# Performance work log

Measured on AMD Instinct MI355X. Metric: run time of the kernel, lower is better.

The kernel has to match this reference:

```python
import jax, jax.numpy as jnp
import numpy as np

N_HEADS = 16

def setup_inputs() -> dict:
    key = jax.random.key(0)
    ks = jax.random.split(key, 5)
    B, T, C = 4, 2048, 1024
    s = 0.02
    return {
        "x": jax.random.normal(ks[0], (B, T, C), jnp.float32),
        "W_attn": jax.random.normal(ks[1], (C, 3 * C), jnp.float32) * s,
        "b_attn": jax.random.normal(ks[2], (3 * C,), jnp.float32) * s,
        "W_proj": jax.random.normal(ks[3], (C, C), jnp.float32) * s,
        "b_proj": jax.random.normal(ks[4], (C,), jnp.float32) * s,
    }

def reference(x, W_attn, b_attn, W_proj, b_proj):
    B, T, C = x.shape
    H = N_HEADS
    D = C // H  # head dim
    qkv = x @ W_attn + b_attn                      # [B,T,3C]
    q, k, v = jnp.split(qkv, 3, axis=2)
    # [B,T,C] -> [B,H,T,D]
    q = q.reshape(B, T, H, D).transpose(0, 2, 1, 3)
    k = k.reshape(B, T, H, D).transpose(0, 2, 1, 3)
    v = v.reshape(B, T, H, D).transpose(0, 2, 1, 3)
    scale = 1.0 / jnp.sqrt(jnp.asarray(D, q.dtype))
    attn = jnp.einsum("bhqd,bhkd->bhqk", q, k) * scale  # [B,H,T,T]
    causal = jnp.tril(jnp.ones((T, T), bool))
    attn = jnp.where(causal[None, None], attn, -jnp.inf)
    attn = jax.nn.softmax(attn, axis=-1)
    y = jnp.einsum("bhqk,bhkd->bhqd", attn, v)          # [B,H,T,D]
    y = y.transpose(0, 2, 1, 3).reshape(B, T, C)
    return y @ W_proj + b_proj
```

## Files before the change

### kernel.cpp

```cpp
#include <hip/hip_runtime.h>

typedef __bf16 bf16x8 __attribute__((ext_vector_type(8)));
typedef float f32x4 __attribute__((ext_vector_type(4)));
typedef float f32x16 __attribute__((ext_vector_type(16)));
typedef unsigned short ushort8 __attribute__((ext_vector_type(8)));
typedef unsigned int uint4v __attribute__((ext_vector_type(4)));

__device__ __forceinline__ unsigned short f2bf(float f) {
  __bf16 b = (__bf16)f;
  return __builtin_bit_cast(unsigned short, b);
}

__global__ __launch_bounds__(256) void wtrans_kernel(const float* __restrict__ W,
                                                     __bf16* __restrict__ Wt,
                                                     int K, int N) {
  __shared__ float tile[32][33];
  int tx = threadIdx.x, ty = threadIdx.y;
  int n0 = blockIdx.x * 32, k0 = blockIdx.y * 32;
#pragma unroll
  for (int i = 0; i < 32; i += 8)
    tile[ty + i][tx] = W[(size_t)(k0 + ty + i) * N + n0 + tx];
  __syncthreads();
#pragma unroll
  for (int i = 0; i < 32; i += 8)
    Wt[(size_t)(n0 + ty + i) * K + k0 + tx] = (__bf16)tile[tx][ty + i];
}

template <int A_F32, int OUT_F32>
__global__ __launch_bounds__(256) void gemm_bt_kernel(const void* __restrict__ Ap,
                                                      const __bf16* __restrict__ Bt,
                                                      const float* __restrict__ bias,
                                                      void* __restrict__ Cp,
                                                      int M, int N, int K) {
  __shared__ __align__(16) unsigned short As[128][40];
  __shared__ __align__(16) unsigned short Bs[128][40];
  const int tid = threadIdx.x;
  const int lane = tid & 63;
  const int wid = tid >> 6;
  const int lr = lane & 15, lg = lane >> 4;
  const int m0 = blockIdx.y * 128, n0 = blockIdx.x * 128;
  const int wm = (wid >> 1) * 64, wn = (wid & 1) * 64;
  f32x4 acc[4][4] = {};
  for (int k0 = 0; k0 < K; k0 += 32) {
#pragma unroll
    for (int p = 0; p < 2; ++p) {
      int idx = p * 256 + tid;
      int r = idx >> 2, c8 = (idx & 3) * 8;
      if (A_F32) {
        const float* A = (const float*)Ap;
        const float4* s4 = (const float4*)(A + (size_t)(m0 + r) * K + k0 + c8);
        float4 f0 = s4[0], f1 = s4[1];
        ushort8 u = {f2bf(f0.x), f2bf(f0.y), f2bf(f0.z), f2bf(f0.w),
                     f2bf(f1.x), f2bf(f1.y), f2bf(f1.z), f2bf(f1.w)};
        *(ushort8*)&As[r][c8] = u;
      } else {
        const __bf16* A = (const __bf16*)Ap;
        *(ushort8*)&As[r][c8] = *(const ushort8*)(A + (size_t)(m0 + r) * K + k0 + c8);
      }
      *(ushort8*)&Bs[r][c8] = *(const ushort8*)(Bt + (size_t)(n0 + r) * K + k0 + c8);
    }
    __syncthreads();
    bf16x8 af[4], bfr[4];
#pragma unroll
    for (int i = 0; i < 4; ++i) af[i] = *(const bf16x8*)&As[wm + i * 16 + lr][lg * 8];
#pragma unroll
    for (int i = 0; i < 4; ++i) bfr[i] = *(const bf16x8*)&Bs[wn + i * 16 + lr][lg * 8];
#pragma unroll
    for (int i = 0; i < 4; ++i)
#pragma unroll
      for (int jn = 0; jn < 4; ++jn)
        acc[i][jn] = __builtin_amdgcn_mfma_f32_16x16x32_bf16(af[i], bfr[jn], acc[i][jn], 0, 0, 0);
    __syncthreads();
  }
#pragma unroll
  for (int i = 0; i < 4; ++i)
#pragma unroll
    for (int jn = 0; jn < 4; ++jn)
#pragma unroll
      for (int jj = 0; jj < 4; ++jj) {
        int row = m0 + wm + i * 16 + lg * 4 + jj;
        int col = n0 + wn + jn * 16 + lr;
        float v = acc[i][jn][jj] + bias[col];
        if (OUT_F32)
          ((float*)Cp)[(size_t)row * N + col] = v;
        else
          ((unsigned short*)Cp)[(size_t)row * N + col] = f2bf(v);
      }
}

__global__ __launch_bounds__(256) void reshape_qk_kernel(const __bf16* __restrict__ qkv,
                                                         __bf16* __restrict__ Q,
                                                         __bf16* __restrict__ Ko) {
  int tid = blockIdx.x * 256 + threadIdx.x;
  int d8 = tid & 7;
  int t = (tid >> 3) & 2047;
  int h = (tid >> 14) & 15;
  int b = tid >> 18;
  size_t src = (size_t)(b * 2048 + t) * 3072 + h * 64 + d8 * 8;
  size_t dst = (size_t)((b * 16 + h) * 2048 + t) * 64 + d8 * 8;
  *(ushort8*)((unsigned short*)Q + dst) = *(const ushort8*)((const unsigned short*)qkv + src);
  *(ushort8*)((unsigned short*)Ko + dst) =
      *(const ushort8*)((const unsigned short*)qkv + src + 1024);
}

__global__ __launch_bounds__(256) void vtrans_kernel(const __bf16* __restrict__ qkv,
                                                     __bf16* __restrict__ Vt) {
  __shared__ __align__(16) unsigned short tile[64][72];
  int bh = blockIdx.y, b = bh >> 4, h = bh & 15;
  int t0 = blockIdx.x * 64;
  int tid = threadIdx.x;
#pragma unroll
  for (int p = 0; p < 2; ++p) {
    int idx = p * 256 + tid;
    int r = idx >> 3, c8 = (idx & 7) * 8;
    *(ushort8*)&tile[r][c8] = *(const ushort8*)((const unsigned short*)qkv +
                                                (size_t)(b * 2048 + t0 + r) * 3072 + 2048 +
                                                h * 64 + c8);
  }
  __syncthreads();
#pragma unroll
  for (int p = 0; p < 2; ++p) {
    int idx = p * 256 + tid;
    int d = idx >> 3, c8 = (idx & 7) * 8;
    ushort8 u;
#pragma unroll
    for (int i = 0; i < 8; ++i) u[i] = tile[c8 + i][d];
    *(ushort8*)((unsigned short*)Vt + (size_t)(bh * 64 + d) * 2048 + t0 + c8) = u;
  }
}

__global__ __launch_bounds__(256) void attn_kernel(const __bf16* __restrict__ Q,
                                                   const __bf16* __restrict__ Kg,
                                                   const __bf16* __restrict__ Vt,
                                                   __bf16* __restrict__ yb) {
  __shared__ __align__(16) unsigned short Ks[2][64][72];
  __shared__ __align__(16) unsigned short Vs[2][64][72];
  const int bx = blockIdx.x;
  const int qb = 15 - (bx >> 6);
  const int bh = bx & 63;
  const int b = bh >> 4, h = bh & 15;
  const int tid = threadIdx.x, wid = tid >> 6, lane = tid & 63;
  const int lq = lane & 31, hi = lane >> 5;
  const unsigned short* Qh = (const unsigned short*)Q + (size_t)bh * 2048 * 64;
  const unsigned short* Kh = (const unsigned short*)Kg + (size_t)bh * 2048 * 64;
  const unsigned short* Vh = (const unsigned short*)Vt + (size_t)bh * 64 * 2048;
  const int q0w = qb * 128 + wid * 32;
  const int jmax_w = 2 * qb + (wid >> 1);
  const int qrel = (wid & 1) * 32 + lq;
  const int J = 2 * qb + 2;

  bf16x8 qf[4];
#pragma unroll
  for (int dc = 0; dc < 4; ++dc)
    qf[dc] = *(const bf16x8*)(Qh + (size_t)(q0w + lq) * 64 + dc * 16 + hi * 8);

  f32x16 yacc[2] = {};
  float m_r = -1e30f, l_r = 0.f;
  const float sc = 0.125f * 1.44269504f;

  {
#pragma unroll
    for (int p = 0; p < 2; ++p) {
      int idx = p * 256 + tid;
      int r = idx >> 3, c8 = (idx & 7) * 8;
      *(ushort8*)&Ks[0][r][c8] = *(const ushort8*)(Kh + (size_t)r * 64 + c8);
      *(ushort8*)&Vs[0][r][c8] = *(const ushort8*)(Vh + (size_t)r * 2048 + c8);
    }
  }

  for (int j = 0; j < J; ++j) {
    __syncthreads();
    if (j + 1 < J) {
      int bi = (j + 1) & 1;
#pragma unroll
      for (int p = 0; p < 2; ++p) {
        int idx = p * 256 + tid;
        int r = idx >> 3, c8 = (idx & 7) * 8;
        *(ushort8*)&Ks[bi][r][c8] =
            *(const ushort8*)(Kh + (size_t)((j + 1) * 64 + r) * 64 + c8);
        *(ushort8*)&Vs[bi][r][c8] =
            *(const ushort8*)(Vh + (size_t)r * 2048 + (j + 1) * 64 + c8);
      }
    }
    if (j <= jmax_w) {
      const int cb = j & 1;
      f32x16 sa[2];
#pragma unroll
      for (int kt32 = 0; kt32 < 2; ++kt32) {
        f32x16 s = {};
#pragma unroll
        for (int dc = 0; dc < 4; ++dc) {
          bf16x8 kf = *(const bf16x8*)&Ks[cb][kt32 * 32 + lq][dc * 16 + hi * 8];
          s = __builtin_amdgcn_mfma_f32_32x32x16_bf16(kf, qf[dc], s, 0, 0, 0);
        }
        sa[kt32] = s;
      }
      float pmax = -1e30f;
#pragma unroll
      for (int kt32 = 0; kt32 < 2; ++kt32)
#pragma unroll
        for (int reg = 0; reg < 16; ++reg) {
          float v = sa[kt32][reg] * sc;
          int kl = kt32 * 32 + (reg & 3) + 8 * (reg >> 2) + 4 * hi;
          if (j == jmax_w && kl > qrel) v = -1e30f;
          sa[kt32][reg] = v;
          pmax = fmaxf(pmax, v);
        }
      pmax = fmaxf(pmax, __shfl_xor(pmax, 32));
      const bool need = __any(pmax > m_r + 8.f) != 0;
      const float mnew = need ? fmaxf(m_r, pmax) : m_r;
      const float alpha = exp2f(m_r - mnew);
      unsigned int u[2][8];
      float rs = 0.f;
#pragma unroll
      for (int kt32 = 0; kt32 < 2; ++kt32)
#pragma unroll
        for (int r = 0; r < 8; ++r) {
          float p0 = exp2f(sa[kt32][2 * r] - mnew);
          float p1 = exp2f(sa[kt32][2 * r + 1] - mnew);
          rs += p0 + p1;
          unsigned int up;
          asm("v_cvt_pk_bf16_f32 %0, %1, %2" : "=v"(up) : "v"(p0), "v"(p1));
          u[kt32][r] = up;
        }
      rs += __shfl_xor(rs, 32);
      l_r = l_r * alpha + rs;
      m_r = mnew;
      if (need) {
#pragma unroll
        for (int reg = 0; reg < 16; ++reg) {
          int row = (reg & 3) + 8 * (reg >> 2) + 4 * hi;
          float ac = __shfl(alpha, row);
          yacc[0][reg] *= ac;
          yacc[1][reg] *= ac;
        }
      }
#pragma unroll
      for (int kt = 0; kt < 4; ++kt) {
        const int kt32 = kt >> 1, off = 4 * (kt & 1);
        unsigned int a0 = u[kt32][off + 0], a2 = u[kt32][off + 2];
        unsigned int a1 = u[kt32][off + 1], a3 = u[kt32][off + 3];
        asm("v_permlane32_swap_b32 %0, %1" : "+v"(a0), "+v"(a2));
        asm("v_permlane32_swap_b32 %0, %1" : "+v"(a1), "+v"(a3));
        uint4v pav = {a0, a1, a2, a3};
        bf16x8 paf = __builtin_bit_cast(bf16x8, pav);
#pragma unroll
        for (int dt = 0; dt < 2; ++dt) {
          bf16x8 vf = *(const bf16x8*)&Vs[cb][dt * 32 + lq][kt * 16 + hi * 8];
          yacc[dt] = __builtin_amdgcn_mfma_f32_32x32x16_bf16(paf, vf, yacc[dt], 0, 0, 0);
        }
      }
    }
  }
#pragma unroll
  for (int reg = 0; reg < 16; ++reg) {
    int row = (reg & 3) + 8 * (reg >> 2) + 4 * hi;
    float linv = 1.f / __shfl(l_r, row);
    int qg = q0w + row;
#pragma unroll
    for (int dt = 0; dt < 2; ++dt) {
      float v = yacc[dt][reg] * linv;
      ((unsigned short*)yb)[(size_t)(b * 2048 + qg) * 1024 + h * 64 + dt * 32 + lq] = f2bf(v);
    }
  }
}

extern "C" void kernel_launch(void* const* d_in, const int* in_sizes, int n_in,
                              void* d_out, int out_size, void* d_ws, size_t ws_size,
                              hipStream_t stream) {
  const float* x = (const float*)d_in[0];
  const float* W_attn = (const float*)d_in[1];
  const float* b_attn = (const float*)d_in[2];
  const float* W_proj = (const float*)d_in[3];
  const float* b_proj = (const float*)d_in[4];
  float* out = (float*)d_out;
  char* ws = (char*)d_ws;

  size_t off = 0;
  __bf16* WtA = (__bf16*)(ws + off); off += (size_t)3072 * 1024 * 2;
  __bf16* WtP = (__bf16*)(ws + off); off += (size_t)1024 * 1024 * 2;
  __bf16* qkv = (__bf16*)(ws + off); off += (size_t)8192 * 3072 * 2;
  __bf16* Qb  = (__bf16*)(ws + off); off += (size_t)64 * 2048 * 64 * 2;
  __bf16* Kb  = (__bf16*)(ws + off); off += (size_t)64 * 2048 * 64 * 2;
  __bf16* Vtb = (__bf16*)(ws + off); off += (size_t)64 * 2048 * 64 * 2;
  __bf16* yb  = (__bf16*)(ws + off); off += (size_t)8192 * 1024 * 2;
  (void)ws_size; (void)in_sizes; (void)n_in; (void)out_size;

  wtrans_kernel<<<dim3(3072 / 32, 1024 / 32), dim3(32, 8), 0, stream>>>(W_attn, WtA, 1024, 3072);
  wtrans_kernel<<<dim3(1024 / 32, 1024 / 32), dim3(32, 8), 0, stream>>>(W_proj, WtP, 1024, 1024);
  gemm_bt_kernel<1, 0><<<dim3(24, 64), 256, 0, stream>>>(x, WtA, b_attn, qkv, 8192, 3072, 1024);
  reshape_qk_kernel<<<4096, 256, 0, stream>>>(qkv, Qb, Kb);
  vtrans_kernel<<<dim3(32, 64), 256, 0, stream>>>(qkv, Vtb);
  attn_kernel<<<dim3(1024), 256, 0, stream>>>(Qb, Kb, Vtb, yb);
  gemm_bt_kernel<0, 1><<<dim3(8, 64), 256, 0, stream>>>(yb, WtP, b_proj, out, 8192, 1024, 1024);
}
```

Measured before the change: 219.0 us.

## Pre-convert x to bf16 and load GEMM tiles directly into LDS

Adds a separate kernel that converts x to bf16 ahead of time, so both GEMMs read bf16 A operands. The GEMM then stages A and B tiles with global_load_lds direct-to-LDS loads instead of going through registers, and remaps block IDs so neighbouring workgroups spread across XCDs for better L2 locality. The LDS tiles lose their padding, which can cause bank conflicts on fragment reads. The extra conversion pass also costs another read and write of x, and the buffer is shared with y.

```diff
diff --git a/kernel.cpp b/kernel.cpp
--- a/kernel.cpp
+++ b/kernel.cpp
@@ -9,6 +9,21 @@
 __device__ __forceinline__ unsigned short f2bf(float f) {
   __bf16 b = (__bf16)f;
   return __builtin_bit_cast(unsigned short, b);
+}
+
+#define GLOAD_LDS16(g, l)                                              \
+  __builtin_amdgcn_global_load_lds(                                    \
+      (const __attribute__((address_space(1))) void*)(g),              \
+      (__attribute__((address_space(3))) void*)(l), 16, 0, 0)
+
+__global__ __launch_bounds__(256) void f32_to_bf16_kernel(const float* __restrict__ in,
+                                                          __bf16* __restrict__ out) {
+  int i = blockIdx.x * 256 + threadIdx.x;
+  const float4* p = (const float4*)(in + (size_t)i * 8);
+  float4 f0 = p[0], f1 = p[1];
+  ushort8 u = {f2bf(f0.x), f2bf(f0.y), f2bf(f0.z), f2bf(f0.w),
+               f2bf(f1.x), f2bf(f1.y), f2bf(f1.z), f2bf(f1.w)};
+  *(ushort8*)((unsigned short*)out + (size_t)i * 8) = u;
 }
 
 __global__ __launch_bounds__(256) void wtrans_kernel(const float* __restrict__ W,
@@ -26,45 +41,42 @@
     Wt[(size_t)(n0 + ty + i) * K + k0 + tx] = (__bf16)tile[tx][ty + i];
 }
 
-template <int A_F32, int OUT_F32>
-__global__ __launch_bounds__(256) void gemm_bt_kernel(const void* __restrict__ Ap,
+template <int OUT_F32>
+__global__ __launch_bounds__(256) void gemm_bt_kernel(const __bf16* __restrict__ Ab,
                                                       const __bf16* __restrict__ Bt,
                                                       const float* __restrict__ bias,
                                                       void* __restrict__ Cp,
                                                       int M, int N, int K) {
-  __shared__ __align__(16) unsigned short As[128][40];
-  __shared__ __align__(16) unsigned short Bs[128][40];
+  __shared__ __align__(16) unsigned short As[128 * 32];
+  __shared__ __align__(16) unsigned short Bs[128 * 32];
   const int tid = threadIdx.x;
   const int lane = tid & 63;
   const int wid = tid >> 6;
   const int lr = lane & 15, lg = lane >> 4;
-  const int m0 = blockIdx.y * 128, n0 = blockIdx.x * 128;
+  const int gx = gridDim.x;
+  int nwg = gx * gridDim.y;
+  int bid = blockIdx.y * gx + blockIdx.x;
+  if ((nwg & 7) == 0) {
+    int cpx = nwg >> 3;
+    bid = (bid & 7) * cpx + (bid >> 3);
+  }
+  const int m0 = (bid / gx) * 128, n0 = (bid % gx) * 128;
   const int wm = (wid >> 1) * 64, wn = (wid & 1) * 64;
+  const int sr = tid >> 2, sc = (tid & 3) * 8;
+  const unsigned short* Ag = (const unsigned short*)Ab + (size_t)(m0 + sr) * K + sc;
+  const unsigned short* Bg = (const unsigned short*)Bt + (size_t)(n0 + sr) * K + sc;
   f32x4 acc[4][4] = {};
   for (int k0 = 0; k0 < K; k0 += 32) {
-#pragma unroll
-    for (int p = 0; p < 2; ++p) {
-      int idx = p * 256 + tid;
-      int r = idx >> 2, c8 = (idx & 3) * 8;
-      if (A_F32) {
-        const float* A = (const float*)Ap;
-        const float4* s4 = (const float4*)(A + (size_t)(m0 + r) * K + k0 + c8);
-        float4 f0 = s4[0], f1 = s4[1];
-        ushort8 u = {f2bf(f0.x), f2bf(f0.y), f2bf(f0.z), f2bf(f0.w),
-                     f2bf(f1.x), f2bf(f1.y), f2bf(f1.z), f2bf(f1.w)};
-        *(ushort8*)&As[r][c8] = u;
-      } else {
-        const __bf16* A = (const __bf16*)Ap;
-        *(ushort8*)&As[r][c8] = *(const ushort8*)(A + (size_t)(m0 + r) * K + k0 + c8);
-      }
-      *(ushort8*)&Bs[r][c8] = *(const ushort8*)(Bt + (size_t)(n0 + r) * K + k0 + c8);
-    }
+    GLOAD_LDS16(Ag + k0, As + tid * 8);
+    GLOAD_LDS16(Ag + (size_t)64 * K + k0, As + 2048 + tid * 8);
+    GLOAD_LDS16(Bg + k0, Bs + tid * 8);
+    GLOAD_LDS16(Bg + (size_t)64 * K + k0, Bs + 2048 + tid * 8);
     __syncthreads();
     bf16x8 af[4], bfr[4];
 #pragma unroll
-    for (int i = 0; i < 4; ++i) af[i] = *(const bf16x8*)&As[wm + i * 16 + lr][lg * 8];
-#pragma unroll
-    for (int i = 0; i < 4; ++i) bfr[i] = *(const bf16x8*)&Bs[wn + i * 16 + lr][lg * 8];
+    for (int i = 0; i < 4; ++i) af[i] = *(const bf16x8*)&As[(wm + i * 16 + lr) * 32 + lg * 8];
+#pragma unroll
+    for (int i = 0; i < 4; ++i) bfr[i] = *(const bf16x8*)&Bs[(wn + i * 16 + lr) * 32 + lg * 8];
 #pragma unroll
     for (int i = 0; i < 4; ++i)
 #pragma unroll
@@ -283,14 +295,17 @@
   __bf16* Qb  = (__bf16*)(ws + off); off += (size_t)64 * 2048 * 64 * 2;
   __bf16* Kb  = (__bf16*)(ws + off); off += (size_t)64 * 2048 * 64 * 2;
   __bf16* Vtb = (__bf16*)(ws + off); off += (size_t)64 * 2048 * 64 * 2;
-  __bf16* yb  = (__bf16*)(ws + off); off += (size_t)8192 * 1024 * 2;
+  __bf16* xyb = (__bf16*)(ws + off); off += (size_t)8192 * 1024 * 2;
+  __bf16* xb = xyb;
+  __bf16* yb = xyb;
   (void)ws_size; (void)in_sizes; (void)n_in; (void)out_size;
 
+  f32_to_bf16_kernel<<<4096, 256, 0, stream>>>(x, xb);
   wtrans_kernel<<<dim3(3072 / 32, 1024 / 32), dim3(32, 8), 0, stream>>>(W_attn, WtA, 1024, 3072);
   wtrans_kernel<<<dim3(1024 / 32, 1024 / 32), dim3(32, 8), 0, stream>>>(W_proj, WtP, 1024, 1024);
-  gemm_bt_kernel<1, 0><<<dim3(24, 64), 256, 0, stream>>>(x, WtA, b_attn, qkv, 8192, 3072, 1024);
+  gemm_bt_kernel<0><<<dim3(24, 64), 256, 0, stream>>>(xb, WtA, b_attn, qkv, 8192, 3072, 1024);
   reshape_qk_kernel<<<4096, 256, 0, stream>>>(qkv, Qb, Kb);
   vtrans_kernel<<<dim3(32, 64), 256, 0, stream>>>(qkv, Vtb);
   attn_kernel<<<dim3(1024), 256, 0, stream>>>(Qb, Kb, Vtb, yb);
-  gemm_bt_kernel<0, 1><<<dim3(8, 64), 256, 0, stream>>>(yb, WtP, b_proj, out, 8192, 1024, 1024);
-}
+  gemm_bt_kernel<1><<<dim3(8, 64), 256, 0, stream>>>(yb, WtP, b_proj, out, 8192, 1024, 1024);
+}
```

Result: faster. 209.1 us (-4.5%).
